# Performance work log

Hardware: AMD Instinct MI355X
Metric: run time of the kernel (lower is better)

## Reference

```python
import jax, jax.numpy as jnp
import numpy as np

N_NODES = 50000
N_EDGES = 800000
IN_C, OUT_C, EDGE_F, HEADS, HID, FINAL = 8, 16, 8, 4, 64, 128
NEG_SLOPE = 0.2  # PyG GATConv default LeakyReLU slope


def setup_inputs() -> dict:
    key = jax.random.key(0)
    ks = jax.random.split(key, 12)
    s = 0.1
    return {
        "x": jax.random.normal(ks[0], (N_NODES, IN_C), jnp.float32),
        "edge_index": jax.random.randint(ks[1], (2, N_EDGES), 0, N_NODES, jnp.int64),
        "edge_attr": jax.random.normal(ks[2], (N_EDGES, EDGE_F), jnp.float32),
        # NNConv params: root weight, bias, edge-MLP Linear(EDGE_F -> IN_C*OUT_C)
        "ecc_root": jax.random.normal(ks[3], (IN_C, OUT_C), jnp.float32) * s,
        "ecc_bias": jnp.zeros((OUT_C,), jnp.float32),
        "mlp_w": jax.random.normal(ks[4], (EDGE_F, IN_C * OUT_C), jnp.float32) * s,
        "mlp_b": jnp.zeros((IN_C * OUT_C,), jnp.float32),
        # GATConv params
        "gat_lin": jax.random.normal(ks[5], (OUT_C, HEADS * HID), jnp.float32) * s,
        "att_src": jax.random.normal(ks[6], (HEADS, HID), jnp.float32) * s,
        "att_dst": jax.random.normal(ks[7], (HEADS, HID), jnp.float32) * s,
        "gat_bias": jnp.zeros((HEADS * HID,), jnp.float32),
        # final Linear
        "fc_w": jax.random.normal(ks[8], (HEADS * HID, FINAL), jnp.float32) * s,
        "fc_b": jnp.zeros((FINAL,), jnp.float32),
    }


def _forward(x, edge_index, edge_attr, ecc_root, ecc_bias, mlp_w, mlp_b,
             gat_lin, att_src, att_dst, gat_bias, fc_w, fc_b):
    src, dst = edge_index[0], edge_index[1]  # messages flow src -> dst

    # ---- NNConv (edge-conditioned conv), aggr='add' ----
    # per-edge weight matrices [E, IN_C, OUT_C] from edge MLP
    w_e = (edge_attr @ mlp_w + mlp_b).reshape(-1, IN_C, OUT_C)
    msg = jnp.einsum('ei,eio->eo', x[src], w_e)                 # [E, OUT_C]
    agg = jax.ops.segment_sum(msg, dst, num_segments=N_NODES)   # [N, OUT_C]
    h = jax.nn.relu(x @ ecc_root + agg + ecc_bias)              # [N, OUT_C]

    # ---- GATConv (heads concatenated) ----
    g = (h @ gat_lin).reshape(N_NODES, HEADS, HID)              # [N, H, D]
    a_src = jnp.einsum('nhd,hd->nh', g, att_src)                # [N, H]
    a_dst = jnp.einsum('nhd,hd->nh', g, att_dst)
    e = jax.nn.leaky_relu(a_src[src] + a_dst[dst], NEG_SLOPE)   # [E, H]
    # segment softmax over incoming edges of each dst node
    e_max = jax.ops.segment_max(e, dst, num_segments=N_NODES)   # [N, H]
    e_max = jnp.where(jnp.isfinite(e_max), e_max, 0.0)
    e_exp = jnp.exp(e - e_max[dst])                             # [E, H]
    denom = jax.ops.segment_sum(e_exp, dst, num_segments=N_NODES)
    alpha = e_exp / (denom[dst] + 1e-16)                        # [E, H]
    out = jax.ops.segment_sum(alpha[:, :, None] * g[src], dst,
                              num_segments=N_NODES)             # [N, H, D]
    out = jax.nn.relu(out.reshape(N_NODES, HEADS * HID) + gat_bias)

    # ---- final linear ----
    return out @ fc_w + fc_b                                    # [N, FINAL]


def reference(x, edge_index, edge_attr, ecc_root, ecc_bias, mlp_w, mlp_b,
              gat_lin, att_src, att_dst, gat_bias, fc_w, fc_b):
    return _forward(x, edge_index, edge_attr, ecc_root, ecc_bias, mlp_w, mlp_b,
                    gat_lin, att_src, att_dst, gat_bias, fc_w, fc_b)
```

## Files before the change

### kernel.cpp

```cpp
#include <hip/hip_runtime.h>

#define N_NODES 50000
#define N_EDGES 800000
#define IN_C 8
#define OUT_C 16
#define EDGE_F 8
#define HEADS 4
#define HID 64
#define GDIM (HEADS*HID)
#define FINAL 128
#define NEG_SLOPE 0.2f
#define EB ((N_EDGES+255)/256)
#define NBLK 196

__device__ __forceinline__ int clampn(int v) {
    return v < 0 ? 0 : (v >= N_NODES ? N_NODES - 1 : v);
}

__global__ __launch_bounds__(256) void k_histfold(
    const int* __restrict__ dst, int* __restrict__ cnt, int* __restrict__ rnk,
    const float* __restrict__ gat_lin,
    const float* __restrict__ att_src_w, const float* __restrict__ att_dst_w,
    float* __restrict__ wsrc, float* __restrict__ wdst)
{
    if (blockIdx.x < EB) {
        int e = blockIdx.x * 256 + threadIdx.x;
        if (e >= N_EDGES) return;
        rnk[e] = atomicAdd(&cnt[clampn(dst[e])], 1);
    } else {
        int t = threadIdx.x;
        if (t >= 64) return;
        int c = t >> 2, h = t & 3;
        float ws = 0.f, wd = 0.f;
        for (int k = 0; k < HID; k++) {
            float l = gat_lin[c * GDIM + h * HID + k];
            ws += l * att_src_w[h * HID + k];
            wd += l * att_dst_w[h * HID + k];
        }
        wsrc[t] = ws;
        wdst[t] = wd;
    }
}

__global__ __launch_bounds__(256) void k_part(const int* __restrict__ cnt,
                                              int* __restrict__ part)
{
    int i = blockIdx.x * 256 + threadIdx.x;
    int v = (i < N_NODES) ? cnt[i] : 0;
#pragma unroll
    for (int off = 32; off; off >>= 1) v += __shfl_down(v, off);
    __shared__ int ws[4];
    if ((threadIdx.x & 63) == 0) ws[threadIdx.x >> 6] = v;
    __syncthreads();
    if (threadIdx.x == 0) part[blockIdx.x] = ws[0] + ws[1] + ws[2] + ws[3];
}

__global__ __launch_bounds__(256) void k_scan1(const int* __restrict__ part,
                                               int* __restrict__ partscan)
{
    int t = threadIdx.x;
    int v = (t < NBLK) ? part[t] : 0;
    int lane = t & 63, wid = t >> 6;
    int incl = v;
#pragma unroll
    for (int off = 1; off < 64; off <<= 1) {
        int u = __shfl_up(incl, off);
        if (lane >= off) incl += u;
    }
    __shared__ int wsum[4];
    if (lane == 63) wsum[wid] = incl;
    __syncthreads();
    int add = 0;
    for (int w = 0; w < wid; w++) add += wsum[w];
    partscan[t] = incl - v + add;
}

__global__ __launch_bounds__(256) void k_add(const int* __restrict__ cnt,
                                             const int* __restrict__ partscan,
                                             int* __restrict__ offs)
{
    int i = blockIdx.x * 256 + threadIdx.x;
    int v = (i < N_NODES) ? cnt[i] : 0;
    int lane = threadIdx.x & 63, wid = threadIdx.x >> 6;
    int incl = v;
#pragma unroll
    for (int off = 1; off < 64; off <<= 1) {
        int u = __shfl_up(incl, off);
        if (lane >= off) incl += u;
    }
    __shared__ int wsum[4];
    if (lane == 63) wsum[wid] = incl;
    __syncthreads();
    int add = partscan[blockIdx.x];
    for (int w = 0; w < wid; w++) add += wsum[w];
    if (i < N_NODES) offs[i] = incl - v + add;
    if (i == 0) offs[N_NODES] = N_EDGES;
}

__global__ __launch_bounds__(256) void k_scatter(
    const int* __restrict__ src, const int* __restrict__ dst,
    const int* __restrict__ rnk, const int* __restrict__ offs,
    int2* __restrict__ se_csr)
{
    int e = blockIdx.x * 256 + threadIdx.x;
    if (e >= N_EDGES) return;
    int p = offs[clampn(dst[e])] + rnk[e];
    se_csr[p] = make_int2(clampn(src[e]), e);
}

__global__ __launch_bounds__(256) void k2T_wave(
    const float* __restrict__ x,
    const int2* __restrict__ se_csr, const int* __restrict__ offs,
    const float* __restrict__ ea,
    const float* __restrict__ mlp_w, const float* __restrict__ mlp_b,
    const float* __restrict__ ecc_root, const float* __restrict__ ecc_bias,
    const float* __restrict__ wsrc, const float* __restrict__ wdst,
    float* __restrict__ h_tab, float* __restrict__ asrc, float* __restrict__ adst)
{
    __shared__ float smW[64 * 17];
    __shared__ float smb[128];
    __shared__ float sroot[128];
    __shared__ float sbias[16];
    __shared__ float sws[64], swd[64];
    __shared__ float sT[4][64];
    __shared__ float sxs[4][8];

    int t = threadIdx.x;
    for (int idx = t; idx < 1024; idx += 256)
        smW[(idx >> 4) * 17 + (idx & 15)] = mlp_w[idx];
    if (t < 128) smb[t] = mlp_b[t];
    if (t >= 128 && t < 256) sroot[t - 128] = ecc_root[t - 128];
    if (t < 16) sbias[t] = ecc_bias[t];
    if (t >= 32 && t < 96) sws[t - 32] = wsrc[t - 32];
    if (t >= 96 && t < 160) swd[t - 96] = wdst[t - 96];

    int wid = t >> 6, lane = t & 63;
    int n = blockIdx.x * 4 + wid;
    int f = lane >> 3, i = lane & 7;
    int beg = offs[n], end = offs[n + 1];

    float t0 = 0.f, t1 = 0.f, t2 = 0.f, t3 = 0.f, xs = 0.f;
    int j = beg;
    for (; j + 3 < end; j += 4) {
        int2 se0 = se_csr[j],     se1 = se_csr[j + 1];
        int2 se2 = se_csr[j + 2], se3 = se_csr[j + 3];
        float a0 = ea[(size_t)se0.y * EDGE_F + f];
        float a1 = ea[(size_t)se1.y * EDGE_F + f];
        float a2 = ea[(size_t)se2.y * EDGE_F + f];
        float a3 = ea[(size_t)se3.y * EDGE_F + f];
        float x0 = x[se0.x * IN_C + i];
        float x1 = x[se1.x * IN_C + i];
        float x2 = x[se2.x * IN_C + i];
        float x3 = x[se3.x * IN_C + i];
        t0 += a0 * x0; t1 += a1 * x1; t2 += a2 * x2; t3 += a3 * x3;
        xs += (x0 + x1) + (x2 + x3);
    }
    for (; j < end; j++) {
        int2 se = se_csr[j];
        float a = ea[(size_t)se.y * EDGE_F + f];
        float xv = x[se.x * IN_C + i];
        t0 += a * xv;
        xs += xv;
    }
    sT[wid][lane] = (t0 + t1) + (t2 + t3);
    if (f == 0) sxs[wid][i] = xs;
    __syncthreads();

    int o = lane & 15, p = lane >> 4;
    float v = 0.f;
#pragma unroll
    for (int q2 = 0; q2 < 16; q2++) {
        int jj = p * 16 + q2;
        v += smW[jj * 17 + o] * sT[wid][jj];
    }
    v += __shfl_down(v, 32);
    v += __shfl_down(v, 16);

    float hv = 0.f;
    if (lane < 16) {
        float vv = v + sbias[o];
#pragma unroll
        for (int ii = 0; ii < IN_C; ii++) {
            vv += smb[ii * 16 + o] * sxs[wid][ii];
            vv += x[n * IN_C + ii] * sroot[ii * 16 + o];
        }
        hv = fmaxf(vv, 0.f);
        h_tab[n * OUT_C + o] = hv;
    }
    float as = 0.f, ad = 0.f;
    int h2 = lane & 3;
#pragma unroll
    for (int c = 0; c < 16; c++) {
        float hc = __shfl(hv, c);
        as += hc * sws[c * 4 + h2];
        ad += hc * swd[c * 4 + h2];
    }
    if (lane < 4) {
        asrc[n * HEADS + lane] = as;
        adst[n * HEADS + lane] = ad;
    }
}

__global__ __launch_bounds__(256) void k_gatE(
    const int* __restrict__ offs, const int2* __restrict__ se_csr,
    const float* __restrict__ asrc, const float* __restrict__ adst,
    const float* __restrict__ h_tab, float* __restrict__ U_all)
{
    int t = threadIdx.x;
    int wid = t >> 6, lane = t & 63;
    int n = blockIdx.x * 4 + wid;
    int h = lane >> 4, c = lane & 15;
    float adsth = adst[n * HEADS + h];
    int beg = offs[n], end = offs[n + 1];

    float U = 0.f, den = 0.f;
    int j = beg;
    for (; j + 3 < end; j += 4) {
        int s0 = se_csr[j].x,     s1 = se_csr[j + 1].x;
        int s2 = se_csr[j + 2].x, s3 = se_csr[j + 3].x;
        float av0 = asrc[s0 * HEADS + h], av1 = asrc[s1 * HEADS + h];
        float av2 = asrc[s2 * HEADS + h], av3 = asrc[s3 * HEADS + h];
        float h0 = h_tab[s0 * OUT_C + c], h1 = h_tab[s1 * OUT_C + c];
        float h2v = h_tab[s2 * OUT_C + c], h3v = h_tab[s3 * OUT_C + c];
        float v0 = av0 + adsth; v0 = v0 > 0.f ? v0 : NEG_SLOPE * v0;
        float v1 = av1 + adsth; v1 = v1 > 0.f ? v1 : NEG_SLOPE * v1;
        float v2 = av2 + adsth; v2 = v2 > 0.f ? v2 : NEG_SLOPE * v2;
        float v3 = av3 + adsth; v3 = v3 > 0.f ? v3 : NEG_SLOPE * v3;
        float p0 = __expf(v0), p1 = __expf(v1), p2 = __expf(v2), p3 = __expf(v3);
        den += (p0 + p1) + (p2 + p3);
        U += p0 * h0 + p1 * h1 + p2 * h2v + p3 * h3v;
    }
    for (; j < end; j++) {
        int s = se_csr[j].x;
        float av = asrc[s * HEADS + h];
        float hvv = h_tab[s * OUT_C + c];
        float v = av + adsth; v = v > 0.f ? v : NEG_SLOPE * v;
        float pe = __expf(v);
        den += pe;
        U += pe * hvv;
    }
    U_all[(size_t)n * 64 + lane] = U / (den + 1e-16f);
}

#define BM 64
#define BK6 16
__global__ __launch_bounds__(256) void k_fuse(
    const float* __restrict__ U_all, const float* __restrict__ gat_lin,
    const float* __restrict__ gat_bias, const float* __restrict__ fc_w,
    const float* __restrict__ fc_b, float* __restrict__ y)
{
    __shared__ float sU[64 * 68];
    __shared__ float slin[16 * GDIM];
    __shared__ float sA[BK6][BM + 4];
    __shared__ float sW[BK6][FINAL];
    int tid = threadIdx.x;
    int r0 = blockIdx.x * BM;

    for (int idx = tid; idx < 16 * GDIM; idx += 256) slin[idx] = gat_lin[idx];
    {
        int row = tid >> 2, hq = tid & 3;
        int grow = r0 + row;
        float4 ua = make_float4(0.f, 0.f, 0.f, 0.f), ub = ua, uc = ua, ud = ua;
        if (grow < N_NODES) {
            const float* up = &U_all[(size_t)grow * 64 + hq * 16];
            ua = *(const float4*)&up[0];
            ub = *(const float4*)&up[4];
            uc = *(const float4*)&up[8];
            ud = *(const float4*)&up[12];
        }
        float* dp = &sU[row * 68 + hq * 16];
        *(float4*)&dp[0]  = ua;
        *(float4*)&dp[4]  = ub;
        *(float4*)&dp[8]  = uc;
        *(float4*)&dp[12] = ud;
    }
    __syncthreads();

    float acc[8][4];
#pragma unroll
    for (int r = 0; r < 8; r++)
#pragma unroll
        for (int c = 0; c < 4; c++) acc[r][c] = 0.f;

    int ar = tid >> 2;
    int ak = (tid & 3) * 4;
    int tcol = (tid & 31) * 4;
    int trow = (tid >> 5) * 8;

    for (int k0 = 0; k0 < GDIM; k0 += BK6) {
        int h = k0 >> 6;
        float4 bv = *(const float4*)&gat_bias[k0 + ak];
        float g0 = 0.f, g1 = 0.f, g2 = 0.f, g3 = 0.f;
        const float* urow = &sU[ar * 68 + h * 16];
#pragma unroll
        for (int c = 0; c < 16; c++) {
            float ucv = urow[c];
            const float* lp = &slin[c * GDIM + k0 + ak];
            g0 += ucv * lp[0];
            g1 += ucv * lp[1];
            g2 += ucv * lp[2];
            g3 += ucv * lp[3];
        }
        sA[ak + 0][ar] = fmaxf(g0 + bv.x, 0.f);
        sA[ak + 1][ar] = fmaxf(g1 + bv.y, 0.f);
        sA[ak + 2][ar] = fmaxf(g2 + bv.z, 0.f);
        sA[ak + 3][ar] = fmaxf(g3 + bv.w, 0.f);
#pragma unroll
        for (int p = 0; p < 2; p++) {
            int kk = (tid >> 5) + p * 8;
            int c = (tid & 31) * 4;
            *(float4*)&sW[kk][c] = *(const float4*)&fc_w[(size_t)(k0 + kk) * FINAL + c];
        }
        __syncthreads();
#pragma unroll
        for (int kk = 0; kk < BK6; kk++) {
            float4 w = *(const float4*)&sW[kk][tcol];
            float4 a0 = *(const float4*)&sA[kk][trow];
            float4 a1 = *(const float4*)&sA[kk][trow + 4];
            float a[8] = {a0.x, a0.y, a0.z, a0.w, a1.x, a1.y, a1.z, a1.w};
#pragma unroll
            for (int r = 0; r < 8; r++) {
                acc[r][0] += a[r] * w.x;
                acc[r][1] += a[r] * w.y;
                acc[r][2] += a[r] * w.z;
                acc[r][3] += a[r] * w.w;
            }
        }
        __syncthreads();
    }

    float4 fb = *(const float4*)&fc_b[tcol];
#pragma unroll
    for (int r = 0; r < 8; r++) {
        int row = r0 + trow + r;
        if (row < N_NODES) {
            *(float4*)&y[(size_t)row * FINAL + tcol] =
                make_float4(acc[r][0] + fb.x, acc[r][1] + fb.y,
                            acc[r][2] + fb.z, acc[r][3] + fb.w);
        }
    }
}

extern "C" void kernel_launch(void* const* d_in, const int* in_sizes, int n_in,
                              void* d_out, int out_size, void* d_ws, size_t ws_size,
                              hipStream_t stream)
{
    const float* x        = (const float*)d_in[0];
    const int*   ei       = (const int*)d_in[1];
    const float* ea       = (const float*)d_in[2];
    const float* ecc_root = (const float*)d_in[3];
    const float* ecc_bias = (const float*)d_in[4];
    const float* mlp_w    = (const float*)d_in[5];
    const float* mlp_b    = (const float*)d_in[6];
    const float* gat_lin  = (const float*)d_in[7];
    const float* att_src  = (const float*)d_in[8];
    const float* att_dst  = (const float*)d_in[9];
    const float* gat_bias = (const float*)d_in[10];
    const float* fc_w     = (const float*)d_in[11];
    const float* fc_b     = (const float*)d_in[12];
    float* y = (float*)d_out;

    const int* src = ei;
    const int* dst = ei + N_EDGES;

    float* h_tab = (float*)d_ws;
    float* U_all = h_tab + (size_t)N_NODES * OUT_C;
    float* asrc  = U_all + (size_t)N_NODES * 64;
    float* adst  = asrc + (size_t)N_NODES * HEADS;
    float* wsrc  = adst + (size_t)N_NODES * HEADS;
    float* wdst  = wsrc + 64;
    int*   cnt      = (int*)(wdst + 64);
    int*   offs     = cnt + N_NODES;
    int*   part     = offs + N_NODES + 1;
    int*   partscan = part + 256;
    int*   rnk      = partscan + 256;
    int2*  se_csr   = (int2*)(rnk + N_EDGES + 1);

    hipMemsetAsync(cnt, 0, sizeof(int) * N_NODES, stream);

    k_histfold<<<EB + 1, 256, 0, stream>>>(dst, cnt, rnk, gat_lin, att_src, att_dst,
                                           wsrc, wdst);
    k_part    <<<NBLK, 256, 0, stream>>>(cnt, part);
    k_scan1   <<<1, 256, 0, stream>>>(part, partscan);
    k_add     <<<NBLK, 256, 0, stream>>>(cnt, partscan, offs);
    k_scatter <<<EB, 256, 0, stream>>>(src, dst, rnk, offs, se_csr);

    k2T_wave  <<<N_NODES / 4, 256, 0, stream>>>(x, se_csr, offs, ea, mlp_w, mlp_b,
                                                ecc_root, ecc_bias, wsrc, wdst,
                                                h_tab, asrc, adst);
    k_gatE    <<<N_NODES / 4, 256, 0, stream>>>(offs, se_csr, asrc, adst, h_tab, U_all);
    k_fuse    <<<(N_NODES + BM - 1) / BM, 256, 0, stream>>>(U_all, gat_lin, gat_bias,
                                                            fc_w, fc_b, y);
}
```

Before: 318.5 us.

## Shrink k_fuse row tile to 32 and keep U rows in registers

The fused GAT-projection plus final-linear kernel now uses 32-row tiles instead of 64, drops the shared-memory staging of U, and loads each head's 16 U values directly into registers. Each thread now computes 2 hidden columns instead of 4 and a 4x4 output tile instead of 8x4, and launch bounds request higher occupancy. The aim is to cut LDS use and register pressure so more blocks fit per CU and to double the grid for better load balance. In exchange, fc_w tiles are reloaded by twice as many blocks and each block does less work per barrier.

```diff
diff --git a/kernel.cpp b/kernel.cpp
--- a/kernel.cpp
+++ b/kernel.cpp
@@ -242,96 +242,86 @@
     U_all[(size_t)n * 64 + lane] = U / (den + 1e-16f);
 }
 
-#define BM 64
-#define BK6 16
-__global__ __launch_bounds__(256) void k_fuse(
+#define FBM 32
+__global__ __launch_bounds__(256, 5) void k_fuse(
     const float* __restrict__ U_all, const float* __restrict__ gat_lin,
     const float* __restrict__ gat_bias, const float* __restrict__ fc_w,
     const float* __restrict__ fc_b, float* __restrict__ y)
 {
-    __shared__ float sU[64 * 68];
     __shared__ float slin[16 * GDIM];
-    __shared__ float sA[BK6][BM + 4];
-    __shared__ float sW[BK6][FINAL];
+    __shared__ float sA[16][FBM + 4];
+    __shared__ float sW[16][FINAL];
     int tid = threadIdx.x;
-    int r0 = blockIdx.x * BM;
-
-    for (int idx = tid; idx < 16 * GDIM; idx += 256) slin[idx] = gat_lin[idx];
-    {
-        int row = tid >> 2, hq = tid & 3;
-        int grow = r0 + row;
-        float4 ua = make_float4(0.f, 0.f, 0.f, 0.f), ub = ua, uc = ua, ud = ua;
+    int r0 = blockIdx.x * FBM;
+
+    for (int idx = tid; idx < (16 * GDIM) / 4; idx += 256)
+        ((float4*)slin)[idx] = ((const float4*)gat_lin)[idx];
+    __syncthreads();
+
+    int ar  = tid >> 3;
+    int ak  = (tid & 7) * 2;
+    int grow = r0 + ar;
+
+    int tcol = (tid & 31) * 4;
+    int trow = (tid >> 5) * 4;
+
+    float acc[4][4];
+#pragma unroll
+    for (int r = 0; r < 4; r++)
+#pragma unroll
+        for (int c = 0; c < 4; c++) acc[r][c] = 0.f;
+
+    for (int h = 0; h < HEADS; ++h) {
+        float4 ua = make_float4(0.f, 0.f, 0.f, 0.f), ub = ua, uc4 = ua, ud = ua;
         if (grow < N_NODES) {
-            const float* up = &U_all[(size_t)grow * 64 + hq * 16];
-            ua = *(const float4*)&up[0];
-            ub = *(const float4*)&up[4];
-            uc = *(const float4*)&up[8];
-            ud = *(const float4*)&up[12];
-        }
-        float* dp = &sU[row * 68 + hq * 16];
-        *(float4*)&dp[0]  = ua;
-        *(float4*)&dp[4]  = ub;
-        *(float4*)&dp[8]  = uc;
-        *(float4*)&dp[12] = ud;
-    }
-    __syncthreads();
-
-    float acc[8][4];
-#pragma unroll
-    for (int r = 0; r < 8; r++)
-#pragma unroll
-        for (int c = 0; c < 4; c++) acc[r][c] = 0.f;
-
-    int ar = tid >> 2;
-    int ak = (tid & 3) * 4;
-    int tcol = (tid & 31) * 4;
-    int trow = (tid >> 5) * 8;
-
-    for (int k0 = 0; k0 < GDIM; k0 += BK6) {
-        int h = k0 >> 6;
-        float4 bv = *(const float4*)&gat_bias[k0 + ak];
-        float g0 = 0.f, g1 = 0.f, g2 = 0.f, g3 = 0.f;
-        const float* urow = &sU[ar * 68 + h * 16];
-#pragma unroll
-        for (int c = 0; c < 16; c++) {
-            float ucv = urow[c];
-            const float* lp = &slin[c * GDIM + k0 + ak];
-            g0 += ucv * lp[0];
-            g1 += ucv * lp[1];
-            g2 += ucv * lp[2];
-            g3 += ucv * lp[3];
-        }
-        sA[ak + 0][ar] = fmaxf(g0 + bv.x, 0.f);
-        sA[ak + 1][ar] = fmaxf(g1 + bv.y, 0.f);
-        sA[ak + 2][ar] = fmaxf(g2 + bv.z, 0.f);
-        sA[ak + 3][ar] = fmaxf(g3 + bv.w, 0.f);
-#pragma unroll
-        for (int p = 0; p < 2; p++) {
-            int kk = (tid >> 5) + p * 8;
-            int c = (tid & 31) * 4;
-            *(float4*)&sW[kk][c] = *(const float4*)&fc_w[(size_t)(k0 + kk) * FINAL + c];
-        }
-        __syncthreads();
-#pragma unroll
-        for (int kk = 0; kk < BK6; kk++) {
-            float4 w = *(const float4*)&sW[kk][tcol];
-            float4 a0 = *(const float4*)&sA[kk][trow];
-            float4 a1 = *(const float4*)&sA[kk][trow + 4];
-            float a[8] = {a0.x, a0.y, a0.z, a0.w, a1.x, a1.y, a1.z, a1.w};
-#pragma unroll
-            for (int r = 0; r < 8; r++) {
-                acc[r][0] += a[r] * w.x;
-                acc[r][1] += a[r] * w.y;
-                acc[r][2] += a[r] * w.z;
-                acc[r][3] += a[r] * w.w;
+            const float4* up = (const float4*)&U_all[(size_t)grow * 64 + h * 16];
+            ua = up[0]; ub = up[1]; uc4 = up[2]; ud = up[3];
+        }
+        float ureg[16] = {ua.x, ua.y, ua.z, ua.w,  ub.x, ub.y, ub.z, ub.w,
+                          uc4.x, uc4.y, uc4.z, uc4.w,  ud.x, ud.y, ud.z, ud.w};
+
+#pragma unroll
+        for (int tt = 0; tt < 4; ++tt) {
+            int k0 = h * 64 + tt * 16;
+            float b0 = gat_bias[k0 + ak];
+            float b1 = gat_bias[k0 + ak + 1];
+            float g0 = 0.f, g1 = 0.f;
+#pragma unroll
+            for (int c = 0; c < 16; ++c) {
+                const float* lp = &slin[c * GDIM + k0 + ak];
+                g0 += ureg[c] * lp[0];
+                g1 += ureg[c] * lp[1];
             }
-        }
-        __syncthreads();
+            __syncthreads();
+            sA[ak][ar]     = fmaxf(g0 + b0, 0.f);
+            sA[ak + 1][ar] = fmaxf(g1 + b1, 0.f);
+#pragma unroll
+            for (int p = 0; p < 2; ++p) {
+                int kk = (tid >> 5) + p * 8;
+                int cc = (tid & 31) * 4;
+                *(float4*)&sW[kk][cc] =
+                    *(const float4*)&fc_w[(size_t)(k0 + kk) * FINAL + cc];
+            }
+            __syncthreads();
+#pragma unroll
+            for (int kk = 0; kk < 16; ++kk) {
+                float4 w = *(const float4*)&sW[kk][tcol];
+                float4 a = *(const float4*)&sA[kk][trow];
+                float av[4] = {a.x, a.y, a.z, a.w};
+#pragma unroll
+                for (int r = 0; r < 4; r++) {
+                    acc[r][0] += av[r] * w.x;
+                    acc[r][1] += av[r] * w.y;
+                    acc[r][2] += av[r] * w.z;
+                    acc[r][3] += av[r] * w.w;
+                }
+            }
+        }
     }
 
     float4 fb = *(const float4*)&fc_b[tcol];
 #pragma unroll
-    for (int r = 0; r < 8; r++) {
+    for (int r = 0; r < 4; r++) {
         int row = r0 + trow + r;
         if (row < N_NODES) {
             *(float4*)&y[(size_t)row * FINAL + tcol] =
@@ -389,6 +379,6 @@
                                                 ecc_root, ecc_bias, wsrc, wdst,
                                                 h_tab, asrc, adst);
     k_gatE    <<<N_NODES / 4, 256, 0, stream>>>(offs, se_csr, asrc, adst, h_tab, U_all);
-    k_fuse    <<<(N_NODES + BM - 1) / BM, 256, 0, stream>>>(U_all, gat_lin, gat_bias,
-                                                            fc_w, fc_b, y);
-}
+    k_fuse    <<<(N_NODES + FBM - 1) / FBM, 256, 0, stream>>>(U_all, gat_lin, gat_bias,
+                                                              fc_w, fc_b, y);
+}
```

Result: no change. 316.3 us (-0.7%).
